# Kernel optimization log

Hardware: AMD Instinct MI355X
Metric: run time of the kernel (lower is better)

The kernel has to match this reference:

```python
import jax, jax.numpy as jnp
import numpy as np

N_NODES = 50000
N_EDGES = 600000
D = 128          # in_dim == hiddim
C = 40           # n_classes
L = 4            # n GCN layers
EPS = 1e-5       # BatchNorm1d default eps


def setup_inputs() -> dict:
    key = jax.random.key(0)
    ks = jax.random.split(key, 5)
    h = jax.random.normal(ks[0], (N_NODES, D), jnp.float32)
    src = jax.random.randint(ks[1], (N_EDGES,), 0, N_NODES, jnp.int32)
    dst = jax.random.randint(ks[2], (N_EDGES,), 0, N_NODES, jnp.int32)
    # learned parameters
    bn_gamma = jnp.ones((D,), jnp.float32)
    bn_beta = jnp.zeros((D,), jnp.float32)
    W1 = jax.random.normal(ks[3], (D, D), jnp.float32) * (1.0 / np.sqrt(D))
    b1 = jnp.zeros((D,), jnp.float32)
    bn2_gamma = jnp.ones((D,), jnp.float32)
    bn2_beta = jnp.zeros((D,), jnp.float32)
    W2 = jax.random.normal(ks[4], (D, C), jnp.float32) * (1.0 / np.sqrt(D))
    b2 = jnp.zeros((C,), jnp.float32)
    return {"h": h, "src": src, "dst": dst,
            "bn_gamma": bn_gamma, "bn_beta": bn_beta,
            "W1": W1, "b1": b1,
            "bn2_gamma": bn2_gamma, "bn2_beta": bn2_beta,
            "W2": W2, "b2": b2}


def _batchnorm(x, gamma, beta):
    # BatchNorm1d in training mode: biased batch variance over the node axis
    mu = x.mean(axis=0)
    var = x.var(axis=0)
    return (x - mu) * jax.lax.rsqrt(var + EPS) * gamma + beta


def reference(h, src, dst, bn_gamma, bn_beta, W1, b1, bn2_gamma, bn2_beta, W2, b2):
    n = h.shape[0]
    # in-degrees from dst indices, clamped to >= 1 (matches g.in_degrees().clamp(min=1))
    deg = jax.ops.segment_sum(jnp.ones(dst.shape[0], jnp.float32), dst, num_segments=n)
    norm = jax.lax.rsqrt(jnp.maximum(deg, 1.0))[:, None]  # deg^{-0.5}, [N,1]
    # in_feat_dropout = 0.0 -> identity
    for _ in range(L):
        h = h * norm
        # copy_u + sum reducer: scatter-add source features into destination nodes
        h = jax.ops.segment_sum(h[src], dst, num_segments=n)
        h = h * norm
        h = jax.nn.relu(_batchnorm(h, bn_gamma, bn_beta))  # shared BN across layers
    # MultiLinearLayer: Linear -> BN -> Linear (activation=None)
    x = h @ W1 + b1
    x = _batchnorm(x, bn2_gamma, bn2_beta)
    return x @ W2 + b2
```

## Files before the change

kernel.cpp:

```cpp
#include <hip/hip_runtime.h>

#define N_NODESC 50000
#define N_EDGESC 600000
#define DDIM 128
#define NCLASS 40
#define BN_EPS 1e-5f
#define STAT_BLOCKS 196
#define GATHER_BLOCKS 2048

typedef short bhalf8 __attribute__((ext_vector_type(8)));
typedef float f32x4 __attribute__((ext_vector_type(4)));

union ABfrag { bhalf8 v; unsigned short u[8]; uint4 q; };

__device__ inline float bflo(unsigned d) { return __builtin_bit_cast(float, d << 16); }
__device__ inline float bfhi(unsigned d) { return __builtin_bit_cast(float, d & 0xffff0000u); }
__device__ inline unsigned short f2bf(float f) {
    unsigned u = __builtin_bit_cast(unsigned, f);
    u += 0x7fffu + ((u >> 16) & 1u);
    return (unsigned short)(u >> 16);
}

__global__ __launch_bounds__(256) void deg_kernel(const int* __restrict__ dst, int* __restrict__ deg) {
    int e = blockIdx.x * 256 + threadIdx.x;
    if (e < N_EDGESC) atomicAdd(&deg[dst[e]], 1);
}

__global__ __launch_bounds__(256) void norm_kernel(const int* __restrict__ deg, float* __restrict__ nrm) {
    int i = blockIdx.x * 256 + threadIdx.x;
    if (i < N_NODESC) {
        float d = (float)deg[i];
        nrm[i] = rsqrtf(fmaxf(d, 1.0f));
    }
}

__global__ __launch_bounds__(256) void scan1_kernel(const int* __restrict__ deg,
                                                    int* __restrict__ rowptr,
                                                    int* __restrict__ blocksums) {
    __shared__ int sh[256];
    int t = threadIdx.x;
    int i = blockIdx.x * 256 + t;
    int v = (i < N_NODESC) ? deg[i] : 0;
    sh[t] = v;
    __syncthreads();
    #pragma unroll
    for (int off = 1; off < 256; off <<= 1) {
        int tv = (t >= off) ? sh[t - off] : 0;
        __syncthreads();
        sh[t] += tv;
        __syncthreads();
    }
    if (i < N_NODESC) rowptr[i] = sh[t] - v;
    if (t == 255) blocksums[blockIdx.x] = sh[255];
}

__global__ void scan2_kernel(const int* __restrict__ blocksums, int* __restrict__ blockoff) {
    __shared__ int sh[256];
    int t = threadIdx.x;
    int v = (t < STAT_BLOCKS) ? blocksums[t] : 0;
    sh[t] = v;
    __syncthreads();
    #pragma unroll
    for (int off = 1; off < 256; off <<= 1) {
        int tv = (t >= off) ? sh[t - off] : 0;
        __syncthreads();
        sh[t] += tv;
        __syncthreads();
    }
    blockoff[t] = sh[t] - v;
}

__global__ __launch_bounds__(256) void scan3_kernel(int* __restrict__ rowptr,
                                                    const int* __restrict__ blockoff,
                                                    int* __restrict__ cursor) {
    int i = blockIdx.x * 256 + threadIdx.x;
    if (i < N_NODESC) {
        int r = rowptr[i] + blockoff[blockIdx.x];
        rowptr[i] = r;
        cursor[i] = r;
    }
    if (blockIdx.x == 0 && threadIdx.x == 0) rowptr[N_NODESC] = N_EDGESC;
}

__global__ __launch_bounds__(256) void fill_kernel(const int* __restrict__ src,
                                                   const int* __restrict__ dst,
                                                   int* __restrict__ cursor,
                                                   int* __restrict__ csr) {
    int e = blockIdx.x * 256 + threadIdx.x;
    if (e < N_EDGESC) {
        int d = dst[e];
        int p = atomicAdd(&cursor[d], 1);
        csr[p] = src[e];
    }
}

__global__ __launch_bounds__(256) void sortrows_kernel(const int* __restrict__ rowptr,
                                                       int* __restrict__ csr) {
    int i = blockIdx.x * 256 + threadIdx.x;
    if (i >= N_NODESC) return;
    int b = rowptr[i], e = rowptr[i + 1];
    for (int j = b + 1; j < e; j++) {
        int v = csr[j];
        int k = j - 1;
        while (k >= b && csr[k] > v) { csr[k + 1] = csr[k]; k--; }
        csr[k + 1] = v;
    }
}

__global__ __launch_bounds__(256) void hconv_kernel(const float* __restrict__ h,
                                                    unsigned short* __restrict__ out) {
    int i = blockIdx.x * 256 + threadIdx.x;
    if (i < N_NODESC * DDIM / 8) {
        float4 v0 = reinterpret_cast<const float4*>(h)[i * 2];
        float4 v1 = reinterpret_cast<const float4*>(h)[i * 2 + 1];
        uint4 p;
        p.x = (unsigned)f2bf(v0.x) | ((unsigned)f2bf(v0.y) << 16);
        p.y = (unsigned)f2bf(v0.z) | ((unsigned)f2bf(v0.w) << 16);
        p.z = (unsigned)f2bf(v1.x) | ((unsigned)f2bf(v1.y) << 16);
        p.w = (unsigned)f2bf(v1.z) | ((unsigned)f2bf(v1.w) << 16);
        reinterpret_cast<uint4*>(out)[i] = p;
    }
}

__global__ __launch_bounds__(256) void w1prep_kernel(const float* __restrict__ W1,
                                                     unsigned short* __restrict__ W1T) {
    int idx = blockIdx.x * 256 + threadIdx.x;
    if (idx < DDIM * DDIM) {
        int k = idx >> 7, n = idx & 127;
        W1T[n * DDIM + k] = f2bf(W1[idx]);
    }
}

template <bool BN>
__global__ __launch_bounds__(256) void gather_kernel(const unsigned short* __restrict__ in,
                                                     const float* __restrict__ nrm,
                                                     const int* __restrict__ rowptr,
                                                     const int* __restrict__ csr,
                                                     const float* __restrict__ mu,
                                                     const float* __restrict__ rstd,
                                                     const float* __restrict__ gamma,
                                                     const float* __restrict__ beta,
                                                     unsigned short* __restrict__ out) {
    int lane = threadIdx.x & 63;
    int wave = threadIdx.x >> 6;
    int q    = lane >> 4;
    int c    = lane & 15;
    float sc[8], sh[8];
    if (BN) {
        float4 m0 = *reinterpret_cast<const float4*>(mu + c * 8);
        float4 m1 = *reinterpret_cast<const float4*>(mu + c * 8 + 4);
        float4 r0 = *reinterpret_cast<const float4*>(rstd + c * 8);
        float4 r1 = *reinterpret_cast<const float4*>(rstd + c * 8 + 4);
        float4 g0 = *reinterpret_cast<const float4*>(gamma + c * 8);
        float4 g1 = *reinterpret_cast<const float4*>(gamma + c * 8 + 4);
        float4 b0 = *reinterpret_cast<const float4*>(beta + c * 8);
        float4 b1 = *reinterpret_cast<const float4*>(beta + c * 8 + 4);
        sc[0] = r0.x * g0.x; sc[1] = r0.y * g0.y; sc[2] = r0.z * g0.z; sc[3] = r0.w * g0.w;
        sc[4] = r1.x * g1.x; sc[5] = r1.y * g1.y; sc[6] = r1.z * g1.z; sc[7] = r1.w * g1.w;
        sh[0] = b0.x - m0.x * sc[0]; sh[1] = b0.y - m0.y * sc[1];
        sh[2] = b0.z - m0.z * sc[2]; sh[3] = b0.w - m0.w * sc[3];
        sh[4] = b1.x - m1.x * sc[4]; sh[5] = b1.y - m1.y * sc[5];
        sh[6] = b1.z - m1.z * sc[6]; sh[7] = b1.w - m1.w * sc[7];
    }
    for (int i = blockIdx.x * 4 + wave; i < N_NODESC; i += GATHER_BLOCKS * 4) {
        int b = rowptr[i], e = rowptr[i + 1];
        float a[8] = {0.f, 0.f, 0.f, 0.f, 0.f, 0.f, 0.f, 0.f};
        for (int j = b + q; j < e; j += 4) {
            int sidx = csr[j];
            float ns = nrm[sidx];
            uint4 d = reinterpret_cast<const uint4*>(in + (size_t)sidx * DDIM)[c];
            float f[8];
            f[0] = bflo(d.x); f[1] = bfhi(d.x);
            f[2] = bflo(d.y); f[3] = bfhi(d.y);
            f[4] = bflo(d.z); f[5] = bfhi(d.z);
            f[6] = bflo(d.w); f[7] = bfhi(d.w);
            #pragma unroll
            for (int t = 0; t < 8; t++) {
                float v = BN ? fmaxf(f[t] * sc[t] + sh[t], 0.f) : f[t];
                a[t] += v * ns;
            }
        }
        #pragma unroll
        for (int t = 0; t < 8; t++) a[t] += __shfl_xor(a[t], 16);
        #pragma unroll
        for (int t = 0; t < 8; t++) a[t] += __shfl_xor(a[t], 32);
        if (q == 0) {
            float ni = nrm[i];
            uint4 p;
            p.x = (unsigned)f2bf(a[0] * ni) | ((unsigned)f2bf(a[1] * ni) << 16);
            p.y = (unsigned)f2bf(a[2] * ni) | ((unsigned)f2bf(a[3] * ni) << 16);
            p.z = (unsigned)f2bf(a[4] * ni) | ((unsigned)f2bf(a[5] * ni) << 16);
            p.w = (unsigned)f2bf(a[6] * ni) | ((unsigned)f2bf(a[7] * ni) << 16);
            reinterpret_cast<uint4*>(out + (size_t)i * DDIM)[c] = p;
        }
    }
}

__global__ __launch_bounds__(256) void stats_bf16_kernel(const unsigned short* __restrict__ x,
                                                         float* __restrict__ partials) {
    __shared__ float sh[256];
    int c2 = threadIdx.x & 63;
    int rg = threadIdx.x >> 6;
    int row0 = blockIdx.x * 256;
    int rowEnd = row0 + 256; if (rowEnd > N_NODESC) rowEnd = N_NODESC;
    float s0 = 0.f, s1 = 0.f, q0 = 0.f, q1 = 0.f;
    for (int r = row0 + rg; r < rowEnd; r += 4) {
        unsigned d = reinterpret_cast<const unsigned*>(x + (size_t)r * DDIM)[c2];
        float f0 = bflo(d), f1 = bfhi(d);
        s0 += f0; q0 += f0 * f0;
        s1 += f1; q1 += f1 * f1;
    }
    sh[threadIdx.x] = s0; __syncthreads();
    if (rg == 0) s0 += sh[64 + c2] + sh[128 + c2] + sh[192 + c2];
    __syncthreads();
    sh[threadIdx.x] = s1; __syncthreads();
    if (rg == 0) s1 += sh[64 + c2] + sh[128 + c2] + sh[192 + c2];
    __syncthreads();
    sh[threadIdx.x] = q0; __syncthreads();
    if (rg == 0) q0 += sh[64 + c2] + sh[128 + c2] + sh[192 + c2];
    __syncthreads();
    sh[threadIdx.x] = q1; __syncthreads();
    if (rg == 0) {
        q1 += sh[64 + c2] + sh[128 + c2] + sh[192 + c2];
        partials[blockIdx.x * 256 + 2 * c2]           = s0;
        partials[blockIdx.x * 256 + 2 * c2 + 1]       = s1;
        partials[blockIdx.x * 256 + 128 + 2 * c2]     = q0;
        partials[blockIdx.x * 256 + 128 + 2 * c2 + 1] = q1;
    }
}

__global__ __launch_bounds__(256) void stats_f32_kernel(const float* __restrict__ x,
                                                        float* __restrict__ partials) {
    __shared__ float sh[256];
    int col = threadIdx.x & 127;
    int grp = threadIdx.x >> 7;
    int rowEnd = (blockIdx.x + 1) * 256;
    if (rowEnd > N_NODESC) rowEnd = N_NODESC;
    float s = 0.f, q = 0.f;
    for (int r = blockIdx.x * 256 + grp; r < rowEnd; r += 2) {
        float v = x[(size_t)r * DDIM + col];
        s += v;
        q += v * v;
    }
    sh[threadIdx.x] = s;
    __syncthreads();
    float s2 = (grp == 0) ? (s + sh[128 + col]) : 0.f;
    __syncthreads();
    sh[threadIdx.x] = q;
    __syncthreads();
    if (grp == 0) {
        float q2 = q + sh[128 + col];
        partials[blockIdx.x * 256 + col]       = s2;
        partials[blockIdx.x * 256 + 128 + col] = q2;
    }
}

__global__ __launch_bounds__(1024) void finalize_kernel(const float* __restrict__ partials,
                                                        float* __restrict__ mu, float* __restrict__ rstd) {
    __shared__ double shd[2048];
    int col = threadIdx.x & 127;
    int sl  = threadIdx.x >> 7;
    double s = 0.0, q = 0.0;
    for (int b = sl; b < STAT_BLOCKS; b += 8) {
        s += (double)partials[b * 256 + col];
        q += (double)partials[b * 256 + 128 + col];
    }
    shd[threadIdx.x] = s;
    shd[1024 + threadIdx.x] = q;
    __syncthreads();
    if (sl == 0) {
        #pragma unroll
        for (int k = 1; k < 8; k++) {
            s += shd[k * 128 + col];
            q += shd[1024 + k * 128 + col];
        }
        double m = s / (double)N_NODESC;
        double v = q / (double)N_NODESC - m * m;
        if (v < 0.0) v = 0.0;
        mu[col]   = (float)m;
        rstd[col] = rsqrtf((float)v + BN_EPS);
    }
}

__global__ __launch_bounds__(256) void linear1_mfma(const unsigned short* __restrict__ Qb,
                                                    const unsigned short* __restrict__ W1T,
                                                    const float* __restrict__ b1,
                                                    const float* __restrict__ mu,
                                                    const float* __restrict__ rstd,
                                                    const float* __restrict__ gamma,
                                                    const float* __restrict__ beta,
                                                    float* __restrict__ X) {
    __shared__ uint4 wlds[2048];
    __shared__ float scs[DDIM], shs[DDIM], bias[DDIM];
    int tid = threadIdx.x;
    for (int i = tid; i < 2048; i += 256) {
        uint4 v = reinterpret_cast<const uint4*>(W1T)[i];
        int o = i << 4;
        int n = o >> 8;
        int sw = (o & 255) ^ ((n & 7) << 4);
        wlds[(n << 4) | (sw >> 4)] = v;
    }
    if (tid < DDIM) {
        float a = rstd[tid] * gamma[tid];
        scs[tid] = a;
        shs[tid] = beta[tid] - mu[tid] * a;
        bias[tid] = b1[tid];
    }
    __syncthreads();
    int wave = tid >> 6, lane = tid & 63;
    int l15 = lane & 15, l4 = lane >> 4;
    int tile = blockIdx.x * 4 + wave;
    if (tile >= 3128) return;
    int row0 = tile * 16;
    int arow = row0 + l15; if (arow >= N_NODESC) arow = N_NODESC - 1;
    const uint4* aptr = reinterpret_cast<const uint4*>(Qb + (size_t)arow * DDIM);
    f32x4 acc[8];
    #pragma unroll
    for (int cf = 0; cf < 8; cf++) acc[cf] = (f32x4){0.f, 0.f, 0.f, 0.f};
    #pragma unroll
    for (int ks = 0; ks < 4; ks++) {
        uint4 ad = aptr[ks * 4 + l4];
        int kb = ks * 32 + l4 * 8;
        ABfrag a;
        float f;
        f = bflo(ad.x); a.u[0] = f2bf(fmaxf(f * scs[kb + 0] + shs[kb + 0], 0.f));
        f = bfhi(ad.x); a.u[1] = f2bf(fmaxf(f * scs[kb + 1] + shs[kb + 1], 0.f));
        f = bflo(ad.y); a.u[2] = f2bf(fmaxf(f * scs[kb + 2] + shs[kb + 2], 0.f));
        f = bfhi(ad.y); a.u[3] = f2bf(fmaxf(f * scs[kb + 3] + shs[kb + 3], 0.f));
        f = bflo(ad.z); a.u[4] = f2bf(fmaxf(f * scs[kb + 4] + shs[kb + 4], 0.f));
        f = bfhi(ad.z); a.u[5] = f2bf(fmaxf(f * scs[kb + 5] + shs[kb + 5], 0.f));
        f = bflo(ad.w); a.u[6] = f2bf(fmaxf(f * scs[kb + 6] + shs[kb + 6], 0.f));
        f = bfhi(ad.w); a.u[7] = f2bf(fmaxf(f * scs[kb + 7] + shs[kb + 7], 0.f));
        int koff = ks * 64 + l4 * 16;
        #pragma unroll
        for (int cf = 0; cf < 8; cf++) {
            int n = cf * 16 + l15;
            ABfrag b;
            b.q = wlds[(n << 4) | ((koff ^ ((n & 7) << 4)) >> 4)];
            acc[cf] = __builtin_amdgcn_mfma_f32_16x16x32_bf16(a.v, b.v, acc[cf], 0, 0, 0);
        }
    }
    #pragma unroll
    for (int cf = 0; cf < 8; cf++) {
        int col = cf * 16 + l15;
        float bb = bias[col];
        #pragma unroll
        for (int r = 0; r < 4; r++) {
            int row = row0 + l4 * 4 + r;
            if (row < N_NODESC) X[(size_t)row * DDIM + col] = acc[cf][r] + bb;
        }
    }
}

__global__ void fold_kernel(const float* __restrict__ W2, const float* __restrict__ b2,
                            const float* __restrict__ g2, const float* __restrict__ be2,
                            const float* __restrict__ mu2, const float* __restrict__ rstd2,
                            float* __restrict__ W2f, float* __restrict__ b2f) {
    __shared__ float s[DDIM], t[DDIM];
    int tid = threadIdx.x;
    if (tid < DDIM) {
        float sc = rstd2[tid] * g2[tid];
        s[tid] = sc;
        t[tid] = be2[tid] - mu2[tid] * sc;
    }
    __syncthreads();
    for (int idx = tid; idx < DDIM * NCLASS; idx += 256) {
        int k = idx / NCLASS;
        W2f[idx] = W2[idx] * s[k];
    }
    if (tid < NCLASS) {
        float acc = b2[tid];
        for (int k = 0; k < DDIM; k++) acc += t[k] * W2[k * NCLASS + tid];
        b2f[tid] = acc;
    }
}

#define L2_TILE 64
__global__ __launch_bounds__(256) void linear2_kernel(const float* __restrict__ X,
                                                      const float* __restrict__ W2f,
                                                      const float* __restrict__ b2f,
                                                      float* __restrict__ out) {
    __shared__ float Ws[DDIM][NCLASS];
    for (int idx = threadIdx.x; idx < DDIM * NCLASS; idx += 256) {
        (&Ws[0][0])[idx] = W2f[idx];
    }
    __syncthreads();
    int cg = threadIdx.x & 7;
    int rp = threadIdx.x >> 3;
    int c0 = cg * 5;
    for (int base = blockIdx.x * L2_TILE; base < N_NODESC; base += gridDim.x * L2_TILE) {
        int row0 = base + rp * 2;
        int row1 = row0 + 1;
        int r0c = row0 < N_NODESC ? row0 : (N_NODESC - 1);
        int r1c = row1 < N_NODESC ? row1 : (N_NODESC - 1);
        const float* r0p = X + (size_t)r0c * DDIM;
        const float* r1p = X + (size_t)r1c * DDIM;
        float a0[5] = {0.f, 0.f, 0.f, 0.f, 0.f};
        float a1[5] = {0.f, 0.f, 0.f, 0.f, 0.f};
        #pragma unroll 4
        for (int k4 = 0; k4 < DDIM; k4 += 4) {
            float4 x0 = *reinterpret_cast<const float4*>(r0p + k4);
            float4 x1 = *reinterpret_cast<const float4*>(r1p + k4);
            #pragma unroll
            for (int j = 0; j < 5; j++) {
                float w0 = Ws[k4 + 0][c0 + j];
                float w1 = Ws[k4 + 1][c0 + j];
                float w2 = Ws[k4 + 2][c0 + j];
                float w3 = Ws[k4 + 3][c0 + j];
                a0[j] += w0 * x0.x + w1 * x0.y + w2 * x0.z + w3 * x0.w;
                a1[j] += w0 * x1.x + w1 * x1.y + w2 * x1.z + w3 * x1.w;
            }
        }
        if (row0 < N_NODESC) {
            #pragma unroll
            for (int j = 0; j < 5; j++) out[(size_t)row0 * NCLASS + c0 + j] = a0[j] + b2f[c0 + j];
        }
        if (row1 < N_NODESC) {
            #pragma unroll
            for (int j = 0; j < 5; j++) out[(size_t)row1 * NCLASS + c0 + j] = a1[j] + b2f[c0 + j];
        }
    }
}

extern "C" void kernel_launch(void* const* d_in, const int* in_sizes, int n_in,
                              void* d_out, int out_size, void* d_ws, size_t ws_size,
                              hipStream_t stream) {
    const float* h    = (const float*)d_in[0];
    const int*   src  = (const int*)d_in[1];
    const int*   dst  = (const int*)d_in[2];
    const float* bn_g = (const float*)d_in[3];
    const float* bn_b = (const float*)d_in[4];
    const float* W1   = (const float*)d_in[5];
    const float* b1   = (const float*)d_in[6];
    const float* g2   = (const float*)d_in[7];
    const float* be2  = (const float*)d_in[8];
    const float* W2   = (const float*)d_in[9];
    const float* b2   = (const float*)d_in[10];
    float* out = (float*)d_out;

    float* ws      = (float*)d_ws;
    float* nrm     = ws;
    int*   deg     = (int*)(ws + N_NODESC);
    int*   cursor  = deg + N_NODESC;
    int*   rowptr  = cursor + N_NODESC;
    int*   bsums   = rowptr + 50016;
    int*   boff    = bsums + 256;
    int*   csr     = boff + 256;
    float* partials = (float*)(csr + N_EDGESC);
    float* mu      = partials + STAT_BLOCKS * 256;
    float* rstd    = mu + DDIM;
    float* W2f     = rstd + DDIM;
    float* b2f     = W2f + DDIM * NCLASS;
    unsigned short* W1T = (unsigned short*)(b2f + 64);
    unsigned short* Hb  = (unsigned short*)((float*)W1T + 8192);
    unsigned short* Pb  = (unsigned short*)((float*)Hb + 3200000);
    float* X       = (float*)((float*)Pb + 3200000);

    (void)in_sizes; (void)n_in; (void)out_size; (void)ws_size;

    hipMemsetAsync(deg, 0, N_NODESC * sizeof(int), stream);
    deg_kernel<<<(N_EDGESC + 255) / 256, 256, 0, stream>>>(dst, deg);
    norm_kernel<<<(N_NODESC + 255) / 256, 256, 0, stream>>>(deg, nrm);
    scan1_kernel<<<STAT_BLOCKS, 256, 0, stream>>>(deg, rowptr, bsums);
    scan2_kernel<<<1, 256, 0, stream>>>(bsums, boff);
    scan3_kernel<<<STAT_BLOCKS, 256, 0, stream>>>(rowptr, boff, cursor);
    fill_kernel<<<(N_EDGESC + 255) / 256, 256, 0, stream>>>(src, dst, cursor, csr);
    sortrows_kernel<<<STAT_BLOCKS, 256, 0, stream>>>(rowptr, csr);
    hconv_kernel<<<(N_NODESC * DDIM / 8 + 255) / 256, 256, 0, stream>>>(h, Hb);
    w1prep_kernel<<<(DDIM * DDIM + 255) / 256, 256, 0, stream>>>(W1, W1T);

    gather_kernel<false><<<GATHER_BLOCKS, 256, 0, stream>>>(Hb, nrm, rowptr, csr,
                                                            nullptr, nullptr, nullptr, nullptr, Pb);
    stats_bf16_kernel<<<STAT_BLOCKS, 256, 0, stream>>>(Pb, partials);
    finalize_kernel<<<1, 1024, 0, stream>>>(partials, mu, rstd);
    gather_kernel<true><<<GATHER_BLOCKS, 256, 0, stream>>>(Pb, nrm, rowptr, csr,
                                                           mu, rstd, bn_g, bn_b, Hb);
    stats_bf16_kernel<<<STAT_BLOCKS, 256, 0, stream>>>(Hb, partials);
    finalize_kernel<<<1, 1024, 0, stream>>>(partials, mu, rstd);
    gather_kernel<true><<<GATHER_BLOCKS, 256, 0, stream>>>(Hb, nrm, rowptr, csr,
                                                           mu, rstd, bn_g, bn_b, Pb);
    stats_bf16_kernel<<<STAT_BLOCKS, 256, 0, stream>>>(Pb, partials);
    finalize_kernel<<<1, 1024, 0, stream>>>(partials, mu, rstd);
    gather_kernel<true><<<GATHER_BLOCKS, 256, 0, stream>>>(Pb, nrm, rowptr, csr,
                                                           mu, rstd, bn_g, bn_b, Hb);
    stats_bf16_kernel<<<STAT_BLOCKS, 256, 0, stream>>>(Hb, partials);
    finalize_kernel<<<1, 1024, 0, stream>>>(partials, mu, rstd);

    linear1_mfma<<<782, 256, 0, stream>>>(Hb, W1T, b1, mu, rstd, bn_g, bn_b, X);
    stats_f32_kernel<<<STAT_BLOCKS, 256, 0, stream>>>(X, partials);
    finalize_kernel<<<1, 1024, 0, stream>>>(partials, mu, rstd);
    fold_kernel<<<1, 256, 0, stream>>>(W2, b2, g2, be2, mu, rstd, W2f, b2f);
    linear2_kernel<<<512, 256, 0, stream>>>(X, W2f, b2f, out);
}
```

Baseline: 457.5 us.

## Sort CSR rows in LDS, fuse norm into scan, prefetch gather loads

The per-row insertion sort now stages each 128-row segment of the CSR array in shared memory, with a global-memory fallback when a segment exceeds capacity. This replaces scattered global read-modify-writes with LDS traffic. The degree-norm computation is folded into scan3, which removes one kernel launch. The gather loop is software-pipelined so the next neighbour's index, norm and feature row are loaded before the current one is accumulated, which raises register use.

Result: faster. 429.4 us (-6.1%).

```diff
diff --git a/kernel.cpp b/kernel.cpp
--- a/kernel.cpp
+++ b/kernel.cpp
@@ -7,6 +7,9 @@
 #define BN_EPS 1e-5f
 #define STAT_BLOCKS 196
 #define GATHER_BLOCKS 2048
+#define SORT_ROWS 128
+#define SORT_CAP 2560
+#define SORT_BLOCKS 391
 
 typedef short bhalf8 __attribute__((ext_vector_type(8)));
 typedef float f32x4 __attribute__((ext_vector_type(4)));
@@ -24,14 +27,6 @@
 __global__ __launch_bounds__(256) void deg_kernel(const int* __restrict__ dst, int* __restrict__ deg) {
     int e = blockIdx.x * 256 + threadIdx.x;
     if (e < N_EDGESC) atomicAdd(&deg[dst[e]], 1);
-}
-
-__global__ __launch_bounds__(256) void norm_kernel(const int* __restrict__ deg, float* __restrict__ nrm) {
-    int i = blockIdx.x * 256 + threadIdx.x;
-    if (i < N_NODESC) {
-        float d = (float)deg[i];
-        nrm[i] = rsqrtf(fmaxf(d, 1.0f));
-    }
 }
 
 __global__ __launch_bounds__(256) void scan1_kernel(const int* __restrict__ deg,
@@ -72,12 +67,15 @@
 
 __global__ __launch_bounds__(256) void scan3_kernel(int* __restrict__ rowptr,
                                                     const int* __restrict__ blockoff,
-                                                    int* __restrict__ cursor) {
+                                                    const int* __restrict__ deg,
+                                                    int* __restrict__ cursor,
+                                                    float* __restrict__ nrm) {
     int i = blockIdx.x * 256 + threadIdx.x;
     if (i < N_NODESC) {
         int r = rowptr[i] + blockoff[blockIdx.x];
         rowptr[i] = r;
         cursor[i] = r;
+        nrm[i] = rsqrtf(fmaxf((float)deg[i], 1.0f));
     }
     if (blockIdx.x == 0 && threadIdx.x == 0) rowptr[N_NODESC] = N_EDGESC;
 }
@@ -94,16 +92,40 @@
     }
 }
 
-__global__ __launch_bounds__(256) void sortrows_kernel(const int* __restrict__ rowptr,
+__global__ __launch_bounds__(128) void sortrows_kernel(const int* __restrict__ rowptr,
                                                        int* __restrict__ csr) {
-    int i = blockIdx.x * 256 + threadIdx.x;
-    if (i >= N_NODESC) return;
-    int b = rowptr[i], e = rowptr[i + 1];
-    for (int j = b + 1; j < e; j++) {
-        int v = csr[j];
-        int k = j - 1;
-        while (k >= b && csr[k] > v) { csr[k + 1] = csr[k]; k--; }
-        csr[k + 1] = v;
+    __shared__ int buf[SORT_CAP];
+    int r0 = blockIdx.x * SORT_ROWS;
+    int r1 = r0 + SORT_ROWS; if (r1 > N_NODESC) r1 = N_NODESC;
+    int base = rowptr[r0];
+    int end  = rowptr[r1];
+    int cnt  = end - base;
+    if (cnt <= SORT_CAP) {
+        for (int j = threadIdx.x; j < cnt; j += 128) buf[j] = csr[base + j];
+        __syncthreads();
+        int i = r0 + threadIdx.x;
+        if (i < r1) {
+            int b = rowptr[i] - base, e = rowptr[i + 1] - base;
+            for (int j = b + 1; j < e; j++) {
+                int v = buf[j];
+                int k = j - 1;
+                while (k >= b && buf[k] > v) { buf[k + 1] = buf[k]; k--; }
+                buf[k + 1] = v;
+            }
+        }
+        __syncthreads();
+        for (int j = threadIdx.x; j < cnt; j += 128) csr[base + j] = buf[j];
+    } else {
+        int i = r0 + threadIdx.x;
+        if (i < r1) {
+            int b = rowptr[i], e = rowptr[i + 1];
+            for (int j = b + 1; j < e; j++) {
+                int v = csr[j];
+                int k = j - 1;
+                while (k >= b && csr[k] > v) { csr[k + 1] = csr[k]; k--; }
+                csr[k + 1] = v;
+            }
+        }
     }
 }
 
@@ -165,19 +187,32 @@
     for (int i = blockIdx.x * 4 + wave; i < N_NODESC; i += GATHER_BLOCKS * 4) {
         int b = rowptr[i], e = rowptr[i + 1];
         float a[8] = {0.f, 0.f, 0.f, 0.f, 0.f, 0.f, 0.f, 0.f};
-        for (int j = b + q; j < e; j += 4) {
+        int j = b + q;
+        if (j < e) {
             int sidx = csr[j];
-            float ns = nrm[sidx];
-            uint4 d = reinterpret_cast<const uint4*>(in + (size_t)sidx * DDIM)[c];
-            float f[8];
-            f[0] = bflo(d.x); f[1] = bfhi(d.x);
-            f[2] = bflo(d.y); f[3] = bfhi(d.y);
-            f[4] = bflo(d.z); f[5] = bfhi(d.z);
-            f[6] = bflo(d.w); f[7] = bfhi(d.w);
-            #pragma unroll
-            for (int t = 0; t < 8; t++) {
-                float v = BN ? fmaxf(f[t] * sc[t] + sh[t], 0.f) : f[t];
-                a[t] += v * ns;
+            float ns  = nrm[sidx];
+            uint4 d   = reinterpret_cast<const uint4*>(in + (size_t)sidx * DDIM)[c];
+            for (j += 4;; j += 4) {
+                bool more = (j < e);
+                int nsidx = 0; float nns = 0.f;
+                uint4 nd = make_uint4(0u, 0u, 0u, 0u);
+                if (more) {
+                    nsidx = csr[j];
+                    nns   = nrm[nsidx];
+                    nd    = reinterpret_cast<const uint4*>(in + (size_t)nsidx * DDIM)[c];
+                }
+                float f[8];
+                f[0] = bflo(d.x); f[1] = bfhi(d.x);
+                f[2] = bflo(d.y); f[3] = bfhi(d.y);
+                f[4] = bflo(d.z); f[5] = bfhi(d.z);
+                f[6] = bflo(d.w); f[7] = bfhi(d.w);
+                #pragma unroll
+                for (int t = 0; t < 8; t++) {
+                    float v = BN ? fmaxf(f[t] * sc[t] + sh[t], 0.f) : f[t];
+                    a[t] += v * ns;
+                }
+                if (!more) break;
+                d = nd; ns = nns;
             }
         }
         #pragma unroll
@@ -460,12 +495,11 @@
 
     hipMemsetAsync(deg, 0, N_NODESC * sizeof(int), stream);
     deg_kernel<<<(N_EDGESC + 255) / 256, 256, 0, stream>>>(dst, deg);
-    norm_kernel<<<(N_NODESC + 255) / 256, 256, 0, stream>>>(deg, nrm);
     scan1_kernel<<<STAT_BLOCKS, 256, 0, stream>>>(deg, rowptr, bsums);
     scan2_kernel<<<1, 256, 0, stream>>>(bsums, boff);
-    scan3_kernel<<<STAT_BLOCKS, 256, 0, stream>>>(rowptr, boff, cursor);
+    scan3_kernel<<<STAT_BLOCKS, 256, 0, stream>>>(rowptr, boff, deg, cursor, nrm);
     fill_kernel<<<(N_EDGESC + 255) / 256, 256, 0, stream>>>(src, dst, cursor, csr);
-    sortrows_kernel<<<STAT_BLOCKS, 256, 0, stream>>>(rowptr, csr);
+    sortrows_kernel<<<SORT_BLOCKS, 128, 0, stream>>>(rowptr, csr);
     hconv_kernel<<<(N_NODESC * DDIM / 8 + 255) / 256, 256, 0, stream>>>(h, Hb);
     w1prep_kernel<<<(DDIM * DDIM + 255) / 256, 256, 0, stream>>>(W1, W1T);
 
```
